# Kernel optimization log

Measured on AMD Instinct MI355X. Metric: run time of the kernel, lower is better.

Reference implementation:

```python
import jax, jax.numpy as jnp
import numpy as np

D = 128   # input_dim / num vars
LEAKY_SLOPE = 0.01  # torch F.leaky_relu default


def setup_inputs() -> dict:
    key = jax.random.key(0)
    ks = jax.random.split(key, 7)
    h, o, b = 64, 2, 8192
    scale = 0.05  # keep activations in a sane range
    return {
        "x": jax.random.normal(ks[0], (b, D), jnp.float32),
        "w0": jax.random.normal(ks[1], (D, h, D), jnp.float32) * scale,
        "w1": jax.random.normal(ks[2], (D, h, h), jnp.float32) * scale,
        "w2": jax.random.normal(ks[3], (D, o, h), jnp.float32) * scale,
        "b0": jax.random.normal(ks[4], (D, h), jnp.float32) * scale,
        "b1": jax.random.normal(ks[5], (D, h), jnp.float32) * scale,
        "b2": jax.random.normal(ks[6], (D, o), jnp.float32) * scale,
    }


def reference(x, w0, w1, w2, b0, b1, b2):
    # adjacency: all-ones minus identity (variable t cannot see itself)
    adj = jnp.ones((D, D), x.dtype) - jnp.eye(D, dtype=x.dtype)  # [j? no: (i,j)] symmetric
    # layer 0: out[b,t,i] = sum_j w0[t,i,j] * adj[j,t] * x[b,j]
    # mask the per-variable weights once, then a single contraction (no (t,i,j,b) intermediate)
    w0m = w0 * adj.T[:, None, :]            # (t,i,j); adj symmetric so adj[j,t]==adj[t,j]
    h = jnp.einsum('tij,bj->bti', w0m, x) + b0
    h = jax.nn.leaky_relu(h, LEAKY_SLOPE)
    # layer 1: per-variable dense
    h = jnp.einsum('tij,btj->bti', w1, h) + b1
    h = jax.nn.leaky_relu(h, LEAKY_SLOPE)
    # layer 2 (output, no nonlinearity)
    out = jnp.einsum('tij,btj->bti', w2, h) + b2  # (b, D, output_dim)
    # torch version returns torch.unbind(out, 1); stacked array carries same values
    return out
```

## Files before the change

### kernel.cpp

```cpp
#include <hip/hip_runtime.h>


typedef __bf16 bf16_t;
typedef __bf16 bf16x8 __attribute__((ext_vector_type(8)));
typedef float  f32x4  __attribute__((ext_vector_type(4)));

#define LEAKY 0.01f

#define XB_OFF   0u
#define W0B_OFF  (2048u*1024u)
#define W1B_OFF  (4096u*1024u)
#define W2B_OFF  (5120u*1024u)

__global__ __launch_bounds__(256)
void brickify(const float* __restrict__ x,  const float* __restrict__ w0,
              const float* __restrict__ w1, const float* __restrict__ w2,
              unsigned char* __restrict__ ws)
{
    const int wid  = blockIdx.x * 4 + (threadIdx.x >> 6);
    const int lane = threadIdx.x & 63;
    const int lr = lane & 15, lq = lane >> 4;

    float v[8];
    if (wid < 2048) {
        int bt = wid >> 5, rem = wid & 31, nt = rem >> 2, ks = rem & 3;
        const float* s = x + (size_t)(bt*128 + nt*16 + lr) * 128 + ks*32 + lq*8;
        const float4 a = *(const float4*)s, b = *(const float4*)(s + 4);
        v[0]=a.x; v[1]=a.y; v[2]=a.z; v[3]=a.w;
        v[4]=b.x; v[5]=b.y; v[6]=b.z; v[7]=b.w;
    } else if (wid < 4096) {
        int u = wid - 2048, t = u >> 4, rem = u & 15, it = rem >> 2, ks = rem & 3;
        int k0 = ks*32 + lq*8;
        const float* s = w0 + (size_t)(t*64 + it*16 + lr) * 128 + k0;
        const float4 a = *(const float4*)s, b = *(const float4*)(s + 4);
        v[0]=a.x; v[1]=a.y; v[2]=a.z; v[3]=a.w;
        v[4]=b.x; v[5]=b.y; v[6]=b.z; v[7]=b.w;
        #pragma unroll
        for (int j = 0; j < 8; ++j) if (k0 + j == t) v[j] = 0.f;
    } else if (wid < 5120) {
        int u = wid - 4096, t = u >> 3, rem = u & 7, it = rem >> 1, ks = rem & 1;
        const float* s = w1 + (size_t)(t*64 + it*16 + lr) * 64 + ks*32 + lq*8;
        const float4 a = *(const float4*)s, b = *(const float4*)(s + 4);
        v[0]=a.x; v[1]=a.y; v[2]=a.z; v[3]=a.w;
        v[4]=b.x; v[5]=b.y; v[6]=b.z; v[7]=b.w;
    } else {
        int u = wid - 5120, t = u >> 1, ks = u & 1;
        #pragma unroll
        for (int j = 0; j < 8; ++j) v[j] = 0.f;
        if (lr < 2) {
            const float* s = w2 + (size_t)(t*2 + lr) * 64 + ks*32 + lq*8;
            const float4 a = *(const float4*)s, b = *(const float4*)(s + 4);
            v[0]=a.x; v[1]=a.y; v[2]=a.z; v[3]=a.w;
            v[4]=b.x; v[5]=b.y; v[6]=b.z; v[7]=b.w;
        }
    }
    union { bf16_t h[8]; uint4 q; } pk;
    #pragma unroll
    for (int j = 0; j < 8; ++j) pk.h[j] = (bf16_t)v[j];
    ((uint4*)ws)[(size_t)wid * 64 + lane] = pk.q;
}

__global__ __launch_bounds__(512, 2)
void fused_mlp(const unsigned char* __restrict__ ws,
               const float* __restrict__ b0, const float* __restrict__ b1,
               const float* __restrict__ b2, float* __restrict__ out)
{
    __shared__ __align__(16) unsigned char hsm[16384];
    __shared__ __align__(16) unsigned char h2sm[16384];

    const int tid  = threadIdx.x;
    const int w    = tid >> 6;
    const int lane = tid & 63;
    const int lr = lane & 15, lq = lane >> 4;
    const int g  = blockIdx.x;
    const int t  = blockIdx.y;

    const unsigned char* w0p = ws + W0B_OFF + (size_t)t*16384 + lane*16;
    const unsigned char* w1p = ws + W1B_OFF + (size_t)t*8192  + lane*16;
    const unsigned char* w2p = ws + W2B_OFF + (size_t)t*2048  + lane*16;
    bf16x8 w0f[4][4], w1f[4][2], w2f[2];
    #pragma unroll
    for (int it = 0; it < 4; ++it)
        #pragma unroll
        for (int ks = 0; ks < 4; ++ks)
            w0f[it][ks] = *(const bf16x8*)(w0p + (it*4+ks)*1024);
    #pragma unroll
    for (int it = 0; it < 4; ++it)
        #pragma unroll
        for (int ks = 0; ks < 2; ++ks)
            w1f[it][ks] = *(const bf16x8*)(w1p + (it*2+ks)*1024);
    #pragma unroll
    for (int ks = 0; ks < 2; ++ks)
        w2f[ks] = *(const bf16x8*)(w2p + ks*1024);

    f32x4 b0q[4], b1q[4];
    #pragma unroll
    for (int it = 0; it < 4; ++it) {
        b0q[it] = *(const f32x4*)(b0 + t*64 + it*16 + lq*4);
        b1q[it] = *(const f32x4*)(b1 + t*64 + it*16 + lq*4);
    }
    const float2 b2v = *(const float2*)(b2 + t*2);

    const unsigned char* xp = ws + XB_OFF + lane*16;
    bf16x8 xf[4];
    #pragma unroll
    for (int ks = 0; ks < 4; ++ks)
        xf[ks] = *(const bf16x8*)(xp + (size_t)(((g*8 + 0)*8 + w)*4 + ks)*1024);

    const int wboff = (((lq >> 1) * 16 + lr) * 16) + (lq & 1) * 8;

    for (int s = 0; s < 8; ++s) {
        const int bt = g*8 + s;

        f32x4 acc[4];
        #pragma unroll
        for (int it = 0; it < 4; ++it) acc[it] = b0q[it];

        #pragma unroll
        for (int ks = 0; ks < 4; ++ks)
            #pragma unroll
            for (int it = 0; it < 4; ++it)
                acc[it] = __builtin_amdgcn_mfma_f32_16x16x32_bf16(
                              w0f[it][ks], xf[ks], acc[it], 0, 0, 0);

        {
            const int btn = (s < 7) ? bt + 1 : bt;
            #pragma unroll
            for (int ks = 0; ks < 4; ++ks)
                xf[ks] = *(const bf16x8*)(xp + (size_t)((btn*8 + w)*4 + ks)*1024);
        }

        #pragma unroll
        for (int it = 0; it < 4; ++it) {
            union { bf16_t h[4]; unsigned long long u; } pk;
            #pragma unroll
            for (int r = 0; r < 4; ++r) {
                float u = acc[it][r];
                pk.h[r] = (bf16_t)fmaxf(u, LEAKY * u);
            }
            int off = (w*2 + (it>>1)) * 1024 + (it&1) * 512 + wboff;
            *(unsigned long long*)(hsm + off) = pk.u;
        }

        bf16x8 hf[2];
        #pragma unroll
        for (int ks = 0; ks < 2; ++ks)
            hf[ks] = *(const bf16x8*)(hsm + (w*2 + ks)*1024 + lane*16);

        #pragma unroll
        for (int it = 0; it < 4; ++it) acc[it] = b1q[it];

        #pragma unroll
        for (int ks = 0; ks < 2; ++ks)
            #pragma unroll
            for (int it = 0; it < 4; ++it)
                acc[it] = __builtin_amdgcn_mfma_f32_16x16x32_bf16(
                              w1f[it][ks], hf[ks], acc[it], 0, 0, 0);

        #pragma unroll
        for (int it = 0; it < 4; ++it) {
            union { bf16_t h[4]; unsigned long long u; } pk;
            #pragma unroll
            for (int r = 0; r < 4; ++r) {
                float u = acc[it][r];
                pk.h[r] = (bf16_t)fmaxf(u, LEAKY * u);
            }
            int off = (w*2 + (it>>1)) * 1024 + (it&1) * 512 + wboff;
            *(unsigned long long*)(h2sm + off) = pk.u;
        }

        bf16x8 h2f[2];
        #pragma unroll
        for (int ks = 0; ks < 2; ++ks)
            h2f[ks] = *(const bf16x8*)(h2sm + (w*2 + ks)*1024 + lane*16);

        f32x4 acc2 = (f32x4){0.f, 0.f, 0.f, 0.f};
        #pragma unroll
        for (int ks = 0; ks < 2; ++ks)
            acc2 = __builtin_amdgcn_mfma_f32_16x16x32_bf16(
                       w2f[ks], h2f[ks], acc2, 0, 0, 0);

        if (lq == 0) {
            int row = bt*128 + w*16 + lr;
            float2 o2 = { acc2[0] + b2v.x, acc2[1] + b2v.y };
            *(float2*)(out + (size_t)row*256 + t*2) = o2;
        }
    }
}

extern "C" void kernel_launch(void* const* d_in, const int* in_sizes, int n_in,
                              void* d_out, int out_size, void* d_ws, size_t ws_size,
                              hipStream_t stream) {
    const float* x  = (const float*)d_in[0];
    const float* w0 = (const float*)d_in[1];
    const float* w1 = (const float*)d_in[2];
    const float* w2 = (const float*)d_in[3];
    const float* b0 = (const float*)d_in[4];
    const float* b1 = (const float*)d_in[5];
    const float* b2 = (const float*)d_in[6];
    unsigned char* ws = (unsigned char*)d_ws;
    float* out = (float*)d_out;

    brickify<<<dim3(1344), dim3(256), 0, stream>>>(x, w0, w1, w2, ws);
    fused_mlp<<<dim3(8, 128), dim3(512), 0, stream>>>(ws, b0, b1, b2, out);
}
```

Baseline: 114.0 us.

## Replace layer-2 MFMA with fp32 shuffle reduction and software-pipeline layers 0/1

The output layer (two outputs) now reads w2 directly in fp32 and computes its dot products with FMAs plus cross-lane shuffles. This drops the second LDS round trip, the bf16 repack and a mostly-empty 16x16 MFMA, and removes the w2 bricks from the preprocessing kernel. The batch-tile loop is also skewed so layer 0 of step s overlaps with layer 1 of step s-1, giving the scheduler independent MFMA chains. The cost is a fully unrolled loop with more live registers, which may pressure occupancy.

```diff
diff --git a/kernel.cpp b/kernel.cpp
--- a/kernel.cpp
+++ b/kernel.cpp
@@ -10,12 +10,10 @@
 #define XB_OFF   0u
 #define W0B_OFF  (2048u*1024u)
 #define W1B_OFF  (4096u*1024u)
-#define W2B_OFF  (5120u*1024u)
 
 __global__ __launch_bounds__(256)
 void brickify(const float* __restrict__ x,  const float* __restrict__ w0,
-              const float* __restrict__ w1, const float* __restrict__ w2,
-              unsigned char* __restrict__ ws)
+              const float* __restrict__ w1, unsigned char* __restrict__ ws)
 {
     const int wid  = blockIdx.x * 4 + (threadIdx.x >> 6);
     const int lane = threadIdx.x & 63;
@@ -37,22 +35,12 @@
         v[4]=b.x; v[5]=b.y; v[6]=b.z; v[7]=b.w;
         #pragma unroll
         for (int j = 0; j < 8; ++j) if (k0 + j == t) v[j] = 0.f;
-    } else if (wid < 5120) {
+    } else {
         int u = wid - 4096, t = u >> 3, rem = u & 7, it = rem >> 1, ks = rem & 1;
         const float* s = w1 + (size_t)(t*64 + it*16 + lr) * 64 + ks*32 + lq*8;
         const float4 a = *(const float4*)s, b = *(const float4*)(s + 4);
         v[0]=a.x; v[1]=a.y; v[2]=a.z; v[3]=a.w;
         v[4]=b.x; v[5]=b.y; v[6]=b.z; v[7]=b.w;
-    } else {
-        int u = wid - 5120, t = u >> 1, ks = u & 1;
-        #pragma unroll
-        for (int j = 0; j < 8; ++j) v[j] = 0.f;
-        if (lr < 2) {
-            const float* s = w2 + (size_t)(t*2 + lr) * 64 + ks*32 + lq*8;
-            const float4 a = *(const float4*)s, b = *(const float4*)(s + 4);
-            v[0]=a.x; v[1]=a.y; v[2]=a.z; v[3]=a.w;
-            v[4]=b.x; v[5]=b.y; v[6]=b.z; v[7]=b.w;
-        }
     }
     union { bf16_t h[8]; uint4 q; } pk;
     #pragma unroll
@@ -62,11 +50,11 @@
 
 __global__ __launch_bounds__(512, 2)
 void fused_mlp(const unsigned char* __restrict__ ws,
+               const float* __restrict__ w2,
                const float* __restrict__ b0, const float* __restrict__ b1,
                const float* __restrict__ b2, float* __restrict__ out)
 {
     __shared__ __align__(16) unsigned char hsm[16384];
-    __shared__ __align__(16) unsigned char h2sm[16384];
 
     const int tid  = threadIdx.x;
     const int w    = tid >> 6;
@@ -77,8 +65,7 @@
 
     const unsigned char* w0p = ws + W0B_OFF + (size_t)t*16384 + lane*16;
     const unsigned char* w1p = ws + W1B_OFF + (size_t)t*8192  + lane*16;
-    const unsigned char* w2p = ws + W2B_OFF + (size_t)t*2048  + lane*16;
-    bf16x8 w0f[4][4], w1f[4][2], w2f[2];
+    bf16x8 w0f[4][4], w1f[4][2];
     #pragma unroll
     for (int it = 0; it < 4; ++it)
         #pragma unroll
@@ -89,9 +76,13 @@
         #pragma unroll
         for (int ks = 0; ks < 2; ++ks)
             w1f[it][ks] = *(const bf16x8*)(w1p + (it*2+ks)*1024);
+
+    f32x4 w2v[2][4];
     #pragma unroll
-    for (int ks = 0; ks < 2; ++ks)
-        w2f[ks] = *(const bf16x8*)(w2p + ks*1024);
+    for (int o = 0; o < 2; ++o)
+        #pragma unroll
+        for (int it = 0; it < 4; ++it)
+            w2v[o][it] = *(const f32x4*)(w2 + t*128 + o*64 + it*16 + lq*4);
 
     f32x4 b0q[4], b1q[4];
     #pragma unroll
@@ -105,85 +96,80 @@
     bf16x8 xf[4];
     #pragma unroll
     for (int ks = 0; ks < 4; ++ks)
-        xf[ks] = *(const bf16x8*)(xp + (size_t)(((g*8 + 0)*8 + w)*4 + ks)*1024);
+        xf[ks] = *(const bf16x8*)(xp + (size_t)((g*8*8 + w)*4 + ks)*1024);
 
-    const int wboff = (((lq >> 1) * 16 + lr) * 16) + (lq & 1) * 8;
+    const int wboff = ((lq >> 1) * 16 + lr) * 16 + (lq & 1) * 8;
 
-    for (int s = 0; s < 8; ++s) {
+    bf16x8 hf[2];
+    f32x4  acc1[4];
+
+    #pragma unroll
+    for (int s = 0; s <= 8; ++s) {
         const int bt = g*8 + s;
 
-        f32x4 acc[4];
-        #pragma unroll
-        for (int it = 0; it < 4; ++it) acc[it] = b0q[it];
+        f32x4 acc0[4];
+        if (s < 8) {
+            #pragma unroll
+            for (int it = 0; it < 4; ++it) acc0[it] = b0q[it];
+            #pragma unroll
+            for (int ks = 0; ks < 4; ++ks)
+                #pragma unroll
+                for (int it = 0; it < 4; ++it)
+                    acc0[it] = __builtin_amdgcn_mfma_f32_16x16x32_bf16(
+                                   w0f[it][ks], xf[ks], acc0[it], 0, 0, 0);
+            if (s < 7) {
+                #pragma unroll
+                for (int ks = 0; ks < 4; ++ks)
+                    xf[ks] = *(const bf16x8*)(xp + (size_t)(((bt+1)*8 + w)*4 + ks)*1024);
+            }
+        }
 
-        #pragma unroll
-        for (int ks = 0; ks < 4; ++ks)
+        if (s > 0) {
+            #pragma unroll
+            for (int it = 0; it < 4; ++it) acc1[it] = b1q[it];
+            #pragma unroll
+            for (int ks = 0; ks < 2; ++ks)
+                #pragma unroll
+                for (int it = 0; it < 4; ++it)
+                    acc1[it] = __builtin_amdgcn_mfma_f32_16x16x32_bf16(
+                                   w1f[it][ks], hf[ks], acc1[it], 0, 0, 0);
+        }
+
+        if (s < 8) {
+            #pragma unroll
+            for (int it = 0; it < 4; ++it) {
+                union { bf16_t h[4]; unsigned long long u; } pk;
+                #pragma unroll
+                for (int r = 0; r < 4; ++r) {
+                    float u = acc0[it][r];
+                    pk.h[r] = (bf16_t)fmaxf(u, LEAKY * u);
+                }
+                int off = (w*2 + (it>>1)) * 1024 + (it&1) * 512 + wboff;
+                *(unsigned long long*)(hsm + off) = pk.u;
+            }
+            #pragma unroll
+            for (int ks = 0; ks < 2; ++ks)
+                hf[ks] = *(const bf16x8*)(hsm + (w*2 + ks)*1024 + lane*16);
+        }
+
+        if (s > 0) {
+            float p0 = 0.f, p1 = 0.f;
             #pragma unroll
             for (int it = 0; it < 4; ++it)
-                acc[it] = __builtin_amdgcn_mfma_f32_16x16x32_bf16(
-                              w0f[it][ks], xf[ks], acc[it], 0, 0, 0);
-
-        {
-            const int btn = (s < 7) ? bt + 1 : bt;
-            #pragma unroll
-            for (int ks = 0; ks < 4; ++ks)
-                xf[ks] = *(const bf16x8*)(xp + (size_t)((btn*8 + w)*4 + ks)*1024);
-        }
-
-        #pragma unroll
-        for (int it = 0; it < 4; ++it) {
-            union { bf16_t h[4]; unsigned long long u; } pk;
-            #pragma unroll
-            for (int r = 0; r < 4; ++r) {
-                float u = acc[it][r];
-                pk.h[r] = (bf16_t)fmaxf(u, LEAKY * u);
+                #pragma unroll
+                for (int r = 0; r < 4; ++r) {
+                    float u = acc1[it][r];
+                    u = fmaxf(u, LEAKY * u);
+                    p0 = fmaf(w2v[0][it][r], u, p0);
+                    p1 = fmaf(w2v[1][it][r], u, p1);
+                }
+            p0 += __shfl_xor(p0, 16); p0 += __shfl_xor(p0, 32);
+            p1 += __shfl_xor(p1, 16); p1 += __shfl_xor(p1, 32);
+            if (lq == 0) {
+                int row = (bt - 1)*128 + w*16 + lr;
+                float2 o2 = { p0 + b2v.x, p1 + b2v.y };
+                *(float2*)(out + (size_t)row*256 + t*2) = o2;
             }
-            int off = (w*2 + (it>>1)) * 1024 + (it&1) * 512 + wboff;
-            *(unsigned long long*)(hsm + off) = pk.u;
-        }
-
-        bf16x8 hf[2];
-        #pragma unroll
-        for (int ks = 0; ks < 2; ++ks)
-            hf[ks] = *(const bf16x8*)(hsm + (w*2 + ks)*1024 + lane*16);
-
-        #pragma unroll
-        for (int it = 0; it < 4; ++it) acc[it] = b1q[it];
-
-        #pragma unroll
-        for (int ks = 0; ks < 2; ++ks)
-            #pragma unroll
-            for (int it = 0; it < 4; ++it)
-                acc[it] = __builtin_amdgcn_mfma_f32_16x16x32_bf16(
-                              w1f[it][ks], hf[ks], acc[it], 0, 0, 0);
-
-        #pragma unroll
-        for (int it = 0; it < 4; ++it) {
-            union { bf16_t h[4]; unsigned long long u; } pk;
-            #pragma unroll
-            for (int r = 0; r < 4; ++r) {
-                float u = acc[it][r];
-                pk.h[r] = (bf16_t)fmaxf(u, LEAKY * u);
-            }
-            int off = (w*2 + (it>>1)) * 1024 + (it&1) * 512 + wboff;
-            *(unsigned long long*)(h2sm + off) = pk.u;
-        }
-
-        bf16x8 h2f[2];
-        #pragma unroll
-        for (int ks = 0; ks < 2; ++ks)
-            h2f[ks] = *(const bf16x8*)(h2sm + (w*2 + ks)*1024 + lane*16);
-
-        f32x4 acc2 = (f32x4){0.f, 0.f, 0.f, 0.f};
-        #pragma unroll
-        for (int ks = 0; ks < 2; ++ks)
-            acc2 = __builtin_amdgcn_mfma_f32_16x16x32_bf16(
-                       w2f[ks], h2f[ks], acc2, 0, 0, 0);
-
-        if (lq == 0) {
-            int row = bt*128 + w*16 + lr;
-            float2 o2 = { acc2[0] + b2v.x, acc2[1] + b2v.y };
-            *(float2*)(out + (size_t)row*256 + t*2) = o2;
         }
     }
 }
@@ -201,6 +187,6 @@
     unsigned char* ws = (unsigned char*)d_ws;
     float* out = (float*)d_out;
 
-    brickify<<<dim3(1344), dim3(256), 0, stream>>>(x, w0, w1, w2, ws);
-    fused_mlp<<<dim3(8, 128), dim3(512), 0, stream>>>(ws, b0, b1, b2, out);
+    brickify<<<dim3(1280), dim3(256), 0, stream>>>(x, w0, w1, ws);
+    fused_mlp<<<dim3(8, 128), dim3(512), 0, stream>>>(ws, w2, b0, b1, b2, out);
 }
```

After: 113.3 us. Within noise of the previous version (-0.6%).
